# Kernel tuning notes

Hardware: AMD Instinct MI355X
Metric: run time of the kernel (lower is better)

## Reference

```python
import jax, jax.numpy as jnp
import numpy as np

O, NI, F, D, NN, M = 2048, 16, 4, 128, 8, 8  # outfits, item slots, factors, dim, neighbors, valid slots
D2 = D // 2

def lrelu(x):
    return jax.nn.leaky_relu(x, 0.01)

def mlp2(x, W1, b1, W2, b2):
    # Linear -> LeakyReLU -> Linear -> LeakyReLU (Dropout is identity at inference)
    return lrelu(lrelu(x @ W1 + b1) @ W2 + b2)

def setup_inputs():
    ks = jax.random.split(jax.random.key(0), 16)
    s = 0.05
    pos = jnp.arange(NI)[None, :]
    outfit_items = jnp.where(pos < M, jax.random.randint(ks[0], (O, NI), 0, NI), -1)
    items_neighbor = jax.random.randint(ks[1], (O, NI, NN), -1, NI)
    items_feature = jax.random.normal(ks[2], (O, NI, D), dtype=jnp.float32)
    items_factors = jnp.zeros((O, NI, F, D), dtype=jnp.float32)
    p = {
        'cf_W1': jax.random.normal(ks[3], (F, D, D2)) * s,
        'cf_b1': jnp.zeros((F, D2)),
        'cf_W2': jax.random.normal(ks[4], (F, D2, D)) * s,
        'cf_b2': jnp.zeros((F, D)),
        'f2f_W1': jax.random.normal(ks[5], (D, D)) * s, 'f2f_b1': jnp.zeros((D,)),
        'f2f_W2': jax.random.normal(ks[6], (D, D)) * s, 'f2f_b2': jnp.zeros((D,)),
        'f2i_W1': jax.random.normal(ks[7], (D, D)) * s, 'f2i_b1': jnp.zeros((D,)),
        'f2i_W2': jax.random.normal(ks[8], (D, D)) * s, 'f2i_b2': jnp.zeros((D,)),
        'i2i_W1': jax.random.normal(ks[9], (D, D)) * s, 'i2i_b1': jnp.zeros((D,)),
        'i2i_W2': jax.random.normal(ks[10], (D, D)) * s, 'i2i_b2': jnp.zeros((D,)),
        'o2s_W': jax.random.normal(ks[11], (D, 1)) * s, 'o2s_b': jnp.zeros((1,)),
    }
    return dict(outfit_items=outfit_items, items_feature=items_feature,
                items_neighbor=items_neighbor, items_factors=items_factors, **p)

def _forward(outfit_items, items_feature, items_neighbor, items_factors,
             cf_W1, cf_b1, cf_W2, cf_b2, f2f_W1, f2f_b1, f2f_W2, f2f_b2,
             f2i_W1, f2i_b1, f2i_W2, f2i_b2, i2i_W1, i2i_b1, i2i_W2, i2i_b2,
             o2s_W, o2s_b):
    del items_factors  # creat_factors overwrites every entry in the original
    # --- creat_factors: per-factor 2-layer MLP on every item feature -> [O,NI,F,D]
    h = lrelu(jnp.einsum('oid,fde->oife', items_feature, cf_W1) + cf_b1)
    fac = lrelu(jnp.einsum('oife,fed->oifd', h, cf_W2) + cf_b2)

    # --- inter_factors: sequential over outfit slots; later slots read updated factors
    def outfit_fac(fac_o, oi_o, nbr_o):
        def step(f, i):
            valid = i != -1
            ic = jnp.maximum(i, 0)
            cand = jnp.concatenate([oi_o, nbr_o[ic]])                # [NI+NN]
            cm = (cand != -1) & (cand != i) & valid
            t = f[ic]                                                # [F,D] snapshot
            msg = mlp2(t[None] * f[jnp.maximum(cand, 0)],
                       f2f_W1, f2f_b1, f2f_W2, f2f_b2)               # [NI+NN,F,D]
            add = jnp.sum(jnp.where(cm[:, None, None], msg, 0.0), axis=0)
            return f.at[ic].add(jnp.where(valid, add, 0.0)), None
        f, _ = jax.lax.scan(step, fac_o, oi_o)
        return f
    fac = jax.vmap(outfit_fac)(fac, outfit_items, items_neighbor)

    # --- infer_items: feature[i] += sum_j f2i(fac[i,j]) for outfit members
    g = mlp2(fac, f2i_W1, f2i_b1, f2i_W2, f2i_b2).sum(axis=2)        # [O,NI,D]
    ic = jnp.maximum(outfit_items, 0)
    w = (outfit_items != -1).astype(g.dtype)                          # [O,NI]
    gsel = jnp.take_along_axis(g, ic[..., None], axis=1)
    scat = jax.vmap(lambda gs, idx, ww: jnp.zeros((NI, D), gs.dtype).at[idx].add(ww[:, None] * gs))
    feat = items_feature + scat(gsel, ic, w)

    # --- inter_items: sequential; current value detached (.data in original)
    def outfit_feat(fo_init, oi_o):
        jc = jnp.maximum(oi_o, 0)
        def step(fo, i):
            valid = i != -1
            ic_ = jnp.maximum(i, 0)
            t = jax.lax.stop_gradient(fo[ic_])
            msgs = mlp2(fo[jc], i2i_W1, i2i_b1, i2i_W2, i2i_b2)      # [NI,D]
            m = ((oi_o != -1) & (oi_o != i)).astype(fo.dtype)
            new = t + jnp.sum(m[:, None] * msgs, axis=0)
            return jnp.where(valid, fo.at[ic_].set(new), fo), None
        fo, _ = jax.lax.scan(step, fo_init, oi_o)
        return fo
    feat = jax.vmap(outfit_feat)(feat, outfit_items)

    # --- infer_outfit + score
    fsel = jnp.take_along_axis(feat, ic[..., None], axis=1)
    outfits = jnp.sum(w[..., None] * fsel, axis=1)                    # [O,D]
    scores = jax.nn.sigmoid(outfits @ o2s_W + o2s_b)[:, 0]            # [O]

    # --- com_loss: ||F F^T - I||_F^2 over valid slots (positional mask), / n_outfits
    G = jnp.einsum('oifd,oigd->oifg', fac, fac) - jnp.eye(F, dtype=fac.dtype)
    com = jnp.sum(w * jnp.sum(G * G, axis=(-1, -2))) / O
    return scores, jnp.reshape(com, (1,))

def reference(outfit_items, items_feature, items_neighbor, items_factors,
              cf_W1, cf_b1, cf_W2, cf_b2, f2f_W1, f2f_b1, f2f_W2, f2f_b2,
              f2i_W1, f2i_b1, f2i_W2, f2i_b2, i2i_W1, i2i_b1, i2i_W2, i2i_b2,
              o2s_W, o2s_b):
    return _forward(outfit_items, items_feature, items_neighbor, items_factors,
                    cf_W1, cf_b1, cf_W2, cf_b2, f2f_W1, f2f_b1, f2f_W2, f2f_b2,
                    f2i_W1, f2i_b1, f2i_W2, f2i_b2, i2i_W1, i2i_b1, i2i_W2, i2i_b2,
                    o2s_W, o2s_b)
```

## Files before the change

### kernel.cpp

```cpp
#include <hip/hip_runtime.h>
#include <hip/hip_bf16.h>
#include <math.h>


typedef __attribute__((ext_vector_type(8))) short short8;
typedef __attribute__((ext_vector_type(4))) float f32x4;

#define MFMA16(a, b, c) __builtin_amdgcn_mfma_f32_16x16x32_bf16(a, b, c, 0, 0, 0)

__device__ __forceinline__ float lrelu(float x) { return fmaxf(x, 0.01f * x); }

__device__ __forceinline__ ushort f2bf(float f) {
  unsigned u = __builtin_bit_cast(unsigned, f);
  u += 0x7fffu + ((u >> 16) & 1u);
  return (ushort)(u >> 16);
}
__device__ __forceinline__ float bflo(unsigned u) {
  return __builtin_bit_cast(float, u << 16);
}
__device__ __forceinline__ unsigned pk2(float a, float b) {
  float2 t; t.x = a; t.y = b;
  __hip_bfloat162 h = __float22bfloat162_rn(t);
  unsigned u;
  __builtin_memcpy(&u, &h, 4);
  return u;
}


__global__ __launch_bounds__(256) void prep_weights(
    const float* __restrict__ cfW1, const float* __restrict__ cfW2,
    const float* __restrict__ f2fW1, const float* __restrict__ f2fW2,
    const float* __restrict__ f2iW1, const float* __restrict__ f2iW2,
    const float* __restrict__ i2iW1, const float* __restrict__ i2iW2,
    ushort* __restrict__ ws, float* __restrict__ out) {
  const int idx = (int)(blockIdx.x * 256 + threadIdx.x);
  if (idx == 0) out[2048] = 0.0f;
  float v;
  if (idx < 32768) {
    int f = idx >> 13, r = idx & 8191, n = r >> 7, k = r & 127;
    v = cfW1[f * 8192 + k * 64 + n];
  } else if (idx < 65536) {
    int t = idx - 32768;
    int f = t >> 13, r = t & 8191, n = r >> 6, k = r & 63;
    v = cfW2[f * 8192 + k * 128 + n];
  } else {
    int t = idx - 65536;
    int seg = t >> 14, r = t & 16383, n = r >> 7, k = r & 127;
    const float* W = (seg == 0) ? f2fW1 : (seg == 1) ? f2fW2 :
                     (seg == 2) ? f2iW1 : (seg == 3) ? f2iW2 :
                     (seg == 4) ? i2iW1 : i2iW2;
    v = W[k * 128 + n];
  }
  ws[idx] = f2bf(v);
}

__global__ __launch_bounds__(512, 4) void mfgn_kernel(
    const int* __restrict__ outfit_items,
    const float* __restrict__ items_feature,
    const int* __restrict__ items_neighbor,
    const float* __restrict__ cfb1, const float* __restrict__ cfb2,
    const float* __restrict__ f2fb1, const float* __restrict__ f2fb2,
    const float* __restrict__ f2ib1, const float* __restrict__ f2ib2,
    const float* __restrict__ i2ib1, const float* __restrict__ i2ib2,
    const float* __restrict__ o2sW, const float* __restrict__ o2sb,
    const ushort* __restrict__ wsW,
    float* __restrict__ out)
{
  __shared__ float facL[16 * 528];
  __shared__ ushort prodS[64 * 136] __attribute__((aligned(16)));
  __shared__ ushort hidS[64 * 136] __attribute__((aligned(16)));
  __shared__ ushort featB[16 * 136] __attribute__((aligned(16)));
  __shared__ float redE[8];
  __shared__ int oiL[16];
  __shared__ int clAll[256];
  __shared__ int ncAll[16];
  __shared__ int vslL[16];
  __shared__ int refcntL[16];
  __shared__ int nvsL;

  const int o = blockIdx.x;
  const int tid = (int)threadIdx.x;
  const int lane = tid & 63;
  const int wid = tid >> 6;
  const int n16 = lane & 15;
  const int q = lane >> 4;
  const int kb = q * 8;
  const int col = wid * 16 + n16;

  if (tid < 16) oiL[tid] = outfit_items[o * 16 + tid];
  {
    const int n = tid >> 5, d0 = (tid & 31) * 4;
    float4 v = *(const float4*)(items_feature + o * 2048 + tid * 4);
    uint2 pk; pk.x = pk2(v.x, v.y); pk.y = pk2(v.z, v.w);
    *(uint2*)(featB + n * 136 + d0) = pk;
  }
  if (tid == 0) {
    int cnt = 0;
    for (int s = 0; s < 16; ++s) refcntL[s] = 0;
    for (int s = 0; s < 16; ++s) {
      int v = oiL[s];
      if (v != -1) { vslL[cnt++] = s; refcntL[v]++; }
    }
    nvsL = cnt;
  }
  for (int s = wid; s < 16; s += 8) {
    const int iv = outfit_items[o * 16 + s];
    if (iv == -1) { if (lane == 0) ncAll[s] = 0; continue; }
    int cand = -1;
    if (lane < 24) cand = (lane < 16) ? outfit_items[o * 16 + lane]
                                      : items_neighbor[o * 128 + iv * 8 + (lane - 16)];
    bool ok = (lane < 24) && (cand != -1) && (cand != iv);
    unsigned long long bm = __ballot(ok);
    if (ok) clAll[s * 16 + __popcll(bm & ((1ull << lane) - 1ull))] = cand;
    if (lane == 0) ncAll[s] = (int)__popcll(bm);
  }
  __syncthreads();
  const int nvs = nvsL;

  {
    const int f = wid & 3, half = wid >> 2;
    short8 wA[2][4];
#pragma unroll
    for (int etl = 0; etl < 2; ++etl)
#pragma unroll
      for (int kt = 0; kt < 4; ++kt)
        wA[etl][kt] = *(const short8*)(wsW + (f * 64 + (half * 2 + etl) * 16 + n16) * 128
                                       + kt * 32 + kb);
    f32x4 acc[2];
#pragma unroll
    for (int etl = 0; etl < 2; ++etl)
      acc[etl] = *(const f32x4*)(cfb1 + f * 64 + (half * 2 + etl) * 16 + q * 4);
    for (int kt = 0; kt < 4; ++kt) {
      short8 x = *(const short8*)(featB + n16 * 136 + kt * 32 + kb);
      acc[0] = MFMA16(wA[0][kt], x, acc[0]);
      acc[1] = MFMA16(wA[1][kt], x, acc[1]);
    }
#pragma unroll
    for (int etl = 0; etl < 2; ++etl) {
      float h0 = lrelu(acc[etl][0]), h1 = lrelu(acc[etl][1]);
      float h2 = lrelu(acc[etl][2]), h3 = lrelu(acc[etl][3]);
      uint2 pk; pk.x = pk2(h0, h1); pk.y = pk2(h2, h3);
      *(uint2*)(hidS + (f * 16 + n16) * 136 + (half * 2 + etl) * 16 + q * 4) = pk;
    }
    __syncthreads();
    short8 wB[4][2];
#pragma unroll
    for (int ctl = 0; ctl < 4; ++ctl)
#pragma unroll
      for (int kt = 0; kt < 2; ++kt)
        wB[ctl][kt] = *(const short8*)(wsW + 32768 + (f * 128 + half * 64 + ctl * 16 + n16) * 64
                                       + kt * 32 + kb);
    f32x4 acc2[4];
#pragma unroll
    for (int ctl = 0; ctl < 4; ++ctl) {
      float b2 = cfb2[f * 128 + half * 64 + ctl * 16 + n16];
      acc2[ctl] = (f32x4){b2, b2, b2, b2};
    }
    for (int kt = 0; kt < 2; ++kt) {
      short8 h = *(const short8*)(hidS + (f * 16 + n16) * 136 + kt * 32 + kb);
#pragma unroll
      for (int ctl = 0; ctl < 4; ++ctl) acc2[ctl] = MFMA16(h, wB[ctl][kt], acc2[ctl]);
    }
#pragma unroll
    for (int ctl = 0; ctl < 4; ++ctl) {
      int c = half * 64 + ctl * 16 + n16;
#pragma unroll
      for (int r = 0; r < 4; ++r)
        facL[(q * 4 + r) * 528 + f * 132 + c] = lrelu(acc2[ctl][r]);
    }
    __syncthreads();
  }

  {
    short8 w1f[4], w2f[4];
#pragma unroll
    for (int kt = 0; kt < 4; ++kt) {
      w1f[kt] = *(const short8*)(wsW + 65536 + col * 128 + kt * 32 + kb);
      w2f[kt] = *(const short8*)(wsW + 81920 + col * 128 + kt * 32 + kb);
    }
    const f32x4 b1q = *(const f32x4*)(f2fb1 + wid * 16 + q * 4);
    const float b2v = f2fb2[col];
    const int rS = tid >> 3, kcS = tid & 7;
    const int fS = rS & 3, ciS = rS >> 2;
    const int k0 = kcS * 16;

    for (int u = 0; u < nvs; ++u) {
      const int s = vslL[u];
      const int iv = oiL[s];
      const int nc = ncAll[s];
      if (ciS < nc) {
        const int cit = clAll[s * 16 + ciS];
        const float* tp = facL + iv * 528 + fS * 132;
        const float* cp = facL + cit * 528 + fS * 132;
#pragma unroll
        for (int i2 = 0; i2 < 2; ++i2) {
          const int k = k0 + i2 * 8;
          float4 a0 = *(const float4*)(tp + k), a1 = *(const float4*)(tp + k + 4);
          float4 c0 = *(const float4*)(cp + k), c1 = *(const float4*)(cp + k + 4);
          uint4 u4;
          u4.x = pk2(a0.x * c0.x, a0.y * c0.y); u4.y = pk2(a0.z * c0.z, a0.w * c0.w);
          u4.z = pk2(a1.x * c1.x, a1.y * c1.y); u4.w = pk2(a1.z * c1.z, a1.w * c1.w);
          *(uint4*)(prodS + rS * 136 + k) = u4;
        }
      } else {
        uint4 z; z.x = z.y = z.z = z.w = 0;
        *(uint4*)(prodS + rS * 136 + k0) = z;
        *(uint4*)(prodS + rS * 136 + k0 + 8) = z;
      }
      __syncthreads();
      f32x4 acc[4];
#pragma unroll
      for (int mt = 0; mt < 4; ++mt) acc[mt] = b1q;
      for (int kt = 0; kt < 4; ++kt)
#pragma unroll
        for (int mt = 0; mt < 4; ++mt) {
          short8 x = *(const short8*)(prodS + (mt * 16 + n16) * 136 + kt * 32 + kb);
          acc[mt] = MFMA16(w1f[kt], x, acc[mt]);
        }
#pragma unroll
      for (int mt = 0; mt < 4; ++mt) {
        float h0 = lrelu(acc[mt][0]), h1 = lrelu(acc[mt][1]);
        float h2 = lrelu(acc[mt][2]), h3 = lrelu(acc[mt][3]);
        uint2 pk; pk.x = pk2(h0, h1); pk.y = pk2(h2, h3);
        *(uint2*)(hidS + (mt * 16 + n16) * 136 + wid * 16 + q * 4) = pk;
      }
      __syncthreads();
      f32x4 acc2[4];
#pragma unroll
      for (int mt = 0; mt < 4; ++mt) acc2[mt] = (f32x4){b2v, b2v, b2v, b2v};
      for (int kt = 0; kt < 4; ++kt)
#pragma unroll
        for (int mt = 0; mt < 4; ++mt) {
          short8 h = *(const short8*)(hidS + (mt * 16 + n16) * 136 + kt * 32 + kb);
          acc2[mt] = MFMA16(h, w2f[kt], acc2[mt]);
        }
      float part[4] = {0.f, 0.f, 0.f, 0.f};
#pragma unroll
      for (int mt = 0; mt < 4; ++mt) {
        bool act = (mt * 4 + q) < nc;
        if (act) {
#pragma unroll
          for (int r = 0; r < 4; ++r) part[r] += lrelu(acc2[mt][r]);
        }
      }
#pragma unroll
      for (int r = 0; r < 4; ++r) {
        float v = part[r];
        v += __shfl_xor(v, 16);
        v += __shfl_xor(v, 32);
        part[r] = v;
      }
      if (q == 0) {
#pragma unroll
        for (int r = 0; r < 4; ++r)
          facL[iv * 528 + r * 132 + col] += part[r];
      }
      __syncthreads();
    }
  }

  {
    short8 w1f[4], w2f[4];
#pragma unroll
    for (int kt = 0; kt < 4; ++kt) {
      w1f[kt] = *(const short8*)(wsW + 98304 + col * 128 + kt * 32 + kb);
      w2f[kt] = *(const short8*)(wsW + 114688 + col * 128 + kt * 32 + kb);
    }
    const f32x4 b1q = *(const f32x4*)(f2ib1 + wid * 16 + q * 4);
    const float b2v = f2ib2[col];
    {
      const int r = tid >> 3, kc = tid & 7, k0 = kc * 16;
      const int f = r & 3, item = r >> 2;
      const float* sp = facL + item * 528 + f * 132;
#pragma unroll
      for (int i2 = 0; i2 < 2; ++i2) {
        const int k = k0 + i2 * 8;
        float4 a0 = *(const float4*)(sp + k), a1 = *(const float4*)(sp + k + 4);
        uint4 u;
        u.x = pk2(a0.x, a0.y); u.y = pk2(a0.z, a0.w);
        u.z = pk2(a1.x, a1.y); u.w = pk2(a1.z, a1.w);
        *(uint4*)(prodS + r * 136 + k) = u;
      }
    }
    __syncthreads();
    f32x4 acc[4];
#pragma unroll
    for (int mt = 0; mt < 4; ++mt) acc[mt] = b1q;
    for (int kt = 0; kt < 4; ++kt)
#pragma unroll
      for (int mt = 0; mt < 4; ++mt) {
        short8 x = *(const short8*)(prodS + (mt * 16 + n16) * 136 + kt * 32 + kb);
        acc[mt] = MFMA16(w1f[kt], x, acc[mt]);
      }
#pragma unroll
    for (int mt = 0; mt < 4; ++mt) {
      float h0 = lrelu(acc[mt][0]), h1 = lrelu(acc[mt][1]);
      float h2 = lrelu(acc[mt][2]), h3 = lrelu(acc[mt][3]);
      uint2 pk; pk.x = pk2(h0, h1); pk.y = pk2(h2, h3);
      *(uint2*)(hidS + (mt * 16 + n16) * 136 + wid * 16 + q * 4) = pk;
    }
    __syncthreads();
    f32x4 acc2[4];
#pragma unroll
    for (int mt = 0; mt < 4; ++mt) acc2[mt] = (f32x4){b2v, b2v, b2v, b2v};
    for (int kt = 0; kt < 4; ++kt)
#pragma unroll
      for (int mt = 0; mt < 4; ++mt) {
        short8 h = *(const short8*)(hidS + (mt * 16 + n16) * 136 + kt * 32 + kb);
        acc2[mt] = MFMA16(h, w2f[kt], acc2[mt]);
      }
#pragma unroll
    for (int mt = 0; mt < 4; ++mt) {
      int item = mt * 4 + q;
      float g = 0.f;
#pragma unroll
      for (int r = 0; r < 4; ++r) g += lrelu(acc2[mt][r]);
      int a = item * 136 + col;
      featB[a] = f2bf(bflo((unsigned)featB[a]) + (float)refcntL[item] * g);
    }
    __syncthreads();
  }

  {
    short8 w1f[4], w2f[4];
#pragma unroll
    for (int kt = 0; kt < 4; ++kt) {
      w1f[kt] = *(const short8*)(wsW + 131072 + col * 128 + kt * 32 + kb);
      w2f[kt] = *(const short8*)(wsW + 147456 + col * 128 + kt * 32 + kb);
    }
    const f32x4 b1q = *(const f32x4*)(i2ib1 + wid * 16 + q * 4);
    const float b2v = i2ib2[col];

    for (int u = 0; u < nvs; ++u) {
      const int iv = oiL[vslL[u]];
      f32x4 acc = b1q;
      for (int kt = 0; kt < 4; ++kt) {
        short8 x = *(const short8*)(featB + n16 * 136 + kt * 32 + kb);
        acc = MFMA16(w1f[kt], x, acc);
      }
      {
        float h0 = lrelu(acc[0]), h1 = lrelu(acc[1]);
        float h2 = lrelu(acc[2]), h3 = lrelu(acc[3]);
        uint2 pk; pk.x = pk2(h0, h1); pk.y = pk2(h2, h3);
        *(uint2*)(hidS + n16 * 136 + wid * 16 + q * 4) = pk;
      }
      __syncthreads();
      f32x4 acc2 = (f32x4){b2v, b2v, b2v, b2v};
      for (int kt = 0; kt < 4; ++kt) {
        short8 h = *(const short8*)(hidS + n16 * 136 + kt * 32 + kb);
        acc2 = MFMA16(h, w2f[kt], acc2);
      }
      float part = 0.f;
#pragma unroll
      for (int r = 0; r < 4; ++r) {
        int item = q * 4 + r;
        float w = (item == iv) ? 0.0f : (float)refcntL[item];
        part += w * lrelu(acc2[r]);
      }
      part += __shfl_xor(part, 16);
      part += __shfl_xor(part, 32);
      if (q == 0) {
        int a = iv * 136 + col;
        featB[a] = f2bf(bflo((unsigned)featB[a]) + part);
      }
      __syncthreads();
    }
  }

  if (tid < 128) {
    float sum = 0.0f;
    for (int u = 0; u < nvs; ++u)
      sum += bflo((unsigned)featB[oiL[vslL[u]] * 136 + tid]);
    float v = sum * o2sW[tid];
#pragma unroll
    for (int off = 1; off < 64; off <<= 1) v += __shfl_xor(v, off);
    if (lane == 0) redE[wid] = v;
  }
  __syncthreads();
  if (tid == 0) {
    float t = redE[0] + redE[1] + o2sb[0];
    out[o] = 1.0f / (1.0f + expf(-t));
  }

  {
    const int n = tid >> 5, f = (tid >> 3) & 3, g = (tid >> 1) & 3, h = tid & 1;
    const float* pa = facL + n * 528 + f * 132 + h * 64;
    const float* pb = facL + n * 528 + g * 132 + h * 64;
    float dot = 0.0f;
    for (int i = 0; i < 16; ++i) {
      float4 a = *(const float4*)(pa + i * 4);
      float4 b = *(const float4*)(pb + i * 4);
      dot += a.x * b.x + a.y * b.y + a.z * b.z + a.w * b.w;
    }
    dot += __shfl_xor(dot, 1);
    float v = dot - ((f == g) ? 1.0f : 0.0f);
    float sq = (h == 0 && oiL[n] != -1) ? v * v : 0.0f;
#pragma unroll
    for (int off = 1; off < 64; off <<= 1) sq += __shfl_xor(sq, off);
    __syncthreads();
    if (lane == 0) redE[wid] = sq;
    __syncthreads();
    if (tid == 0) {
      float tot = 0.f;
#pragma unroll
      for (int w = 0; w < 8; ++w) tot += redE[w];
      atomicAdd(out + 2048, tot * (1.0f / 2048.0f));
    }
  }
}

extern "C" void kernel_launch(void* const* d_in, const int* in_sizes, int n_in,
                              void* d_out, int out_size, void* d_ws, size_t ws_size,
                              hipStream_t stream) {
  float* out = (float*)d_out;
  ushort* ws = (ushort*)d_ws;
  hipLaunchKernelGGL(prep_weights, dim3(640), dim3(256), 0, stream,
                     (const float*)d_in[4], (const float*)d_in[6],
                     (const float*)d_in[8], (const float*)d_in[10],
                     (const float*)d_in[12], (const float*)d_in[14],
                     (const float*)d_in[16], (const float*)d_in[18],
                     ws, out);
  hipLaunchKernelGGL(mfgn_kernel, dim3(2048), dim3(512), 0, stream,
                     (const int*)d_in[0],
                     (const float*)d_in[1],
                     (const int*)d_in[2],
                     (const float*)d_in[5], (const float*)d_in[7],
                     (const float*)d_in[9], (const float*)d_in[11],
                     (const float*)d_in[13], (const float*)d_in[15],
                     (const float*)d_in[17], (const float*)d_in[19],
                     (const float*)d_in[20], (const float*)d_in[21],
                     (const ushort*)ws,
                     out);
}
```

Before: 337.2 us.

## Shrink LDS footprint with XOR-swizzled unpadded buffers and merge prod/hidden buffers

Replaces the padded shared-memory layouts with unpadded rows indexed through an XOR swizzle, so bank conflicts stay avoided without padding. It merges the separate product and hidden staging buffers into one and adds barriers to guard the reuse. The neighbor list is stored as bytes, and launch bounds now ask for more resident blocks per CU. The aim is to cut LDS use so more workgroups fit per CU, at the cost of two extra barriers per loop iteration. Zero-filling of unused product rows is also dropped, so those rows feed stale data into columns that are later masked out.

```diff
diff --git a/kernel.cpp b/kernel.cpp
--- a/kernel.cpp
+++ b/kernel.cpp
@@ -24,6 +24,13 @@
   unsigned u;
   __builtin_memcpy(&u, &h, 4);
   return u;
+}
+
+__device__ __forceinline__ int fIdx(int row, int k) {
+  return row * 128 + (k ^ ((row & 7) << 2));
+}
+__device__ __forceinline__ int bIdx(int row, int k) {
+  return row * 128 + (k ^ ((row & 7) << 3));
 }
 
 
@@ -54,7 +61,7 @@
   ws[idx] = f2bf(v);
 }
 
-__global__ __launch_bounds__(512, 4) void mfgn_kernel(
+__global__ __launch_bounds__(512, 6) void mfgn_kernel(
     const int* __restrict__ outfit_items,
     const float* __restrict__ items_feature,
     const int* __restrict__ items_neighbor,
@@ -66,13 +73,12 @@
     const ushort* __restrict__ wsW,
     float* __restrict__ out)
 {
-  __shared__ float facL[16 * 528];
-  __shared__ ushort prodS[64 * 136] __attribute__((aligned(16)));
-  __shared__ ushort hidS[64 * 136] __attribute__((aligned(16)));
-  __shared__ ushort featB[16 * 136] __attribute__((aligned(16)));
+  __shared__ float facL[64 * 128] __attribute__((aligned(16)));
+  __shared__ ushort bufS[64 * 128] __attribute__((aligned(16)));
+  __shared__ ushort featB[16 * 128] __attribute__((aligned(16)));
   __shared__ float redE[8];
   __shared__ int oiL[16];
-  __shared__ int clAll[256];
+  __shared__ unsigned char clAllU[256];
   __shared__ int ncAll[16];
   __shared__ int vslL[16];
   __shared__ int refcntL[16];
@@ -92,7 +98,7 @@
     const int n = tid >> 5, d0 = (tid & 31) * 4;
     float4 v = *(const float4*)(items_feature + o * 2048 + tid * 4);
     uint2 pk; pk.x = pk2(v.x, v.y); pk.y = pk2(v.z, v.w);
-    *(uint2*)(featB + n * 136 + d0) = pk;
+    *(uint2*)(featB + bIdx(n, d0)) = pk;
   }
   if (tid == 0) {
     int cnt = 0;
@@ -111,7 +117,7 @@
                                       : items_neighbor[o * 128 + iv * 8 + (lane - 16)];
     bool ok = (lane < 24) && (cand != -1) && (cand != iv);
     unsigned long long bm = __ballot(ok);
-    if (ok) clAll[s * 16 + __popcll(bm & ((1ull << lane) - 1ull))] = cand;
+    if (ok) clAllU[s * 16 + __popcll(bm & ((1ull << lane) - 1ull))] = (unsigned char)cand;
     if (lane == 0) ncAll[s] = (int)__popcll(bm);
   }
   __syncthreads();
@@ -131,7 +137,7 @@
     for (int etl = 0; etl < 2; ++etl)
       acc[etl] = *(const f32x4*)(cfb1 + f * 64 + (half * 2 + etl) * 16 + q * 4);
     for (int kt = 0; kt < 4; ++kt) {
-      short8 x = *(const short8*)(featB + n16 * 136 + kt * 32 + kb);
+      short8 x = *(const short8*)(featB + bIdx(n16, kt * 32 + kb));
       acc[0] = MFMA16(wA[0][kt], x, acc[0]);
       acc[1] = MFMA16(wA[1][kt], x, acc[1]);
     }
@@ -140,7 +146,7 @@
       float h0 = lrelu(acc[etl][0]), h1 = lrelu(acc[etl][1]);
       float h2 = lrelu(acc[etl][2]), h3 = lrelu(acc[etl][3]);
       uint2 pk; pk.x = pk2(h0, h1); pk.y = pk2(h2, h3);
-      *(uint2*)(hidS + (f * 16 + n16) * 136 + (half * 2 + etl) * 16 + q * 4) = pk;
+      *(uint2*)(bufS + bIdx(f * 16 + n16, (half * 2 + etl) * 16 + q * 4)) = pk;
     }
     __syncthreads();
     short8 wB[4][2];
@@ -157,7 +163,7 @@
       acc2[ctl] = (f32x4){b2, b2, b2, b2};
     }
     for (int kt = 0; kt < 2; ++kt) {
-      short8 h = *(const short8*)(hidS + (f * 16 + n16) * 136 + kt * 32 + kb);
+      short8 h = *(const short8*)(bufS + bIdx(f * 16 + n16, kt * 32 + kb));
 #pragma unroll
       for (int ctl = 0; ctl < 4; ++ctl) acc2[ctl] = MFMA16(h, wB[ctl][kt], acc2[ctl]);
     }
@@ -166,7 +172,7 @@
       int c = half * 64 + ctl * 16 + n16;
 #pragma unroll
       for (int r = 0; r < 4; ++r)
-        facL[(q * 4 + r) * 528 + f * 132 + c] = lrelu(acc2[ctl][r]);
+        facL[fIdx((q * 4 + r) * 4 + f, c)] = lrelu(acc2[ctl][r]);
     }
     __syncthreads();
   }
@@ -189,23 +195,23 @@
       const int iv = oiL[s];
       const int nc = ncAll[s];
       if (ciS < nc) {
-        const int cit = clAll[s * 16 + ciS];
-        const float* tp = facL + iv * 528 + fS * 132;
-        const float* cp = facL + cit * 528 + fS * 132;
+        const int cit = (int)clAllU[s * 16 + ciS];
+        const int rT = iv * 4 + fS, rC = cit * 4 + fS;
+        const int swT = (rT & 7) << 2, swC = (rC & 7) << 2;
+        const float* tp = facL + rT * 128;
+        const float* cp = facL + rC * 128;
 #pragma unroll
         for (int i2 = 0; i2 < 2; ++i2) {
           const int k = k0 + i2 * 8;
-          float4 a0 = *(const float4*)(tp + k), a1 = *(const float4*)(tp + k + 4);
-          float4 c0 = *(const float4*)(cp + k), c1 = *(const float4*)(cp + k + 4);
+          float4 a0 = *(const float4*)(tp + (k ^ swT));
+          float4 a1 = *(const float4*)(tp + ((k + 4) ^ swT));
+          float4 c0 = *(const float4*)(cp + (k ^ swC));
+          float4 c1 = *(const float4*)(cp + ((k + 4) ^ swC));
           uint4 u4;
           u4.x = pk2(a0.x * c0.x, a0.y * c0.y); u4.y = pk2(a0.z * c0.z, a0.w * c0.w);
           u4.z = pk2(a1.x * c1.x, a1.y * c1.y); u4.w = pk2(a1.z * c1.z, a1.w * c1.w);
-          *(uint4*)(prodS + rS * 136 + k) = u4;
+          *(uint4*)(bufS + bIdx(rS, k)) = u4;
         }
-      } else {
-        uint4 z; z.x = z.y = z.z = z.w = 0;
-        *(uint4*)(prodS + rS * 136 + k0) = z;
-        *(uint4*)(prodS + rS * 136 + k0 + 8) = z;
       }
       __syncthreads();
       f32x4 acc[4];
@@ -214,15 +220,16 @@
       for (int kt = 0; kt < 4; ++kt)
 #pragma unroll
         for (int mt = 0; mt < 4; ++mt) {
-          short8 x = *(const short8*)(prodS + (mt * 16 + n16) * 136 + kt * 32 + kb);
+          short8 x = *(const short8*)(bufS + bIdx(mt * 16 + n16, kt * 32 + kb));
           acc[mt] = MFMA16(w1f[kt], x, acc[mt]);
         }
+      __syncthreads();
 #pragma unroll
       for (int mt = 0; mt < 4; ++mt) {
         float h0 = lrelu(acc[mt][0]), h1 = lrelu(acc[mt][1]);
         float h2 = lrelu(acc[mt][2]), h3 = lrelu(acc[mt][3]);
         uint2 pk; pk.x = pk2(h0, h1); pk.y = pk2(h2, h3);
-        *(uint2*)(hidS + (mt * 16 + n16) * 136 + wid * 16 + q * 4) = pk;
+        *(uint2*)(bufS + bIdx(mt * 16 + n16, wid * 16 + q * 4)) = pk;
       }
       __syncthreads();
       f32x4 acc2[4];
@@ -231,7 +238,7 @@
       for (int kt = 0; kt < 4; ++kt)
 #pragma unroll
         for (int mt = 0; mt < 4; ++mt) {
-          short8 h = *(const short8*)(hidS + (mt * 16 + n16) * 136 + kt * 32 + kb);
+          short8 h = *(const short8*)(bufS + bIdx(mt * 16 + n16, kt * 32 + kb));
           acc2[mt] = MFMA16(h, w2f[kt], acc2[mt]);
         }
       float part[4] = {0.f, 0.f, 0.f, 0.f};
@@ -253,7 +260,7 @@
       if (q == 0) {
 #pragma unroll
         for (int r = 0; r < 4; ++r)
-          facL[iv * 528 + r * 132 + col] += part[r];
+          facL[fIdx(iv * 4 + r, col)] += part[r];
       }
       __syncthreads();
     }
@@ -270,16 +277,17 @@
     const float b2v = f2ib2[col];
     {
       const int r = tid >> 3, kc = tid & 7, k0 = kc * 16;
-      const int f = r & 3, item = r >> 2;
-      const float* sp = facL + item * 528 + f * 132;
+      const int sw = (r & 7) << 2;
+      const float* sp = facL + r * 128;
 #pragma unroll
       for (int i2 = 0; i2 < 2; ++i2) {
         const int k = k0 + i2 * 8;
-        float4 a0 = *(const float4*)(sp + k), a1 = *(const float4*)(sp + k + 4);
+        float4 a0 = *(const float4*)(sp + (k ^ sw));
+        float4 a1 = *(const float4*)(sp + ((k + 4) ^ sw));
         uint4 u;
         u.x = pk2(a0.x, a0.y); u.y = pk2(a0.z, a0.w);
         u.z = pk2(a1.x, a1.y); u.w = pk2(a1.z, a1.w);
-        *(uint4*)(prodS + r * 136 + k) = u;
+        *(uint4*)(bufS + bIdx(r, k)) = u;
       }
     }
     __syncthreads();
@@ -289,15 +297,16 @@
     for (int kt = 0; kt < 4; ++kt)
 #pragma unroll
       for (int mt = 0; mt < 4; ++mt) {
-        short8 x = *(const short8*)(prodS + (mt * 16 + n16) * 136 + kt * 32 + kb);
+        short8 x = *(const short8*)(bufS + bIdx(mt * 16 + n16, kt * 32 + kb));
         acc[mt] = MFMA16(w1f[kt], x, acc[mt]);
       }
+    __syncthreads();
 #pragma unroll
     for (int mt = 0; mt < 4; ++mt) {
       float h0 = lrelu(acc[mt][0]), h1 = lrelu(acc[mt][1]);
       float h2 = lrelu(acc[mt][2]), h3 = lrelu(acc[mt][3]);
       uint2 pk; pk.x = pk2(h0, h1); pk.y = pk2(h2, h3);
-      *(uint2*)(hidS + (mt * 16 + n16) * 136 + wid * 16 + q * 4) = pk;
+      *(uint2*)(bufS + bIdx(mt * 16 + n16, wid * 16 + q * 4)) = pk;
     }
     __syncthreads();
     f32x4 acc2[4];
@@ -306,7 +315,7 @@
     for (int kt = 0; kt < 4; ++kt)
 #pragma unroll
       for (int mt = 0; mt < 4; ++mt) {
-        short8 h = *(const short8*)(hidS + (mt * 16 + n16) * 136 + kt * 32 + kb);
+        short8 h = *(const short8*)(bufS + bIdx(mt * 16 + n16, kt * 32 + kb));
         acc2[mt] = MFMA16(h, w2f[kt], acc2[mt]);
       }
 #pragma unroll
@@ -315,7 +324,7 @@
       float g = 0.f;
 #pragma unroll
       for (int r = 0; r < 4; ++r) g += lrelu(acc2[mt][r]);
-      int a = item * 136 + col;
+      int a = bIdx(item, col);
       featB[a] = f2bf(bflo((unsigned)featB[a]) + (float)refcntL[item] * g);
     }
     __syncthreads();
@@ -335,19 +344,19 @@
       const int iv = oiL[vslL[u]];
       f32x4 acc = b1q;
       for (int kt = 0; kt < 4; ++kt) {
-        short8 x = *(const short8*)(featB + n16 * 136 + kt * 32 + kb);
+        short8 x = *(const short8*)(featB + bIdx(n16, kt * 32 + kb));
         acc = MFMA16(w1f[kt], x, acc);
       }
       {
         float h0 = lrelu(acc[0]), h1 = lrelu(acc[1]);
         float h2 = lrelu(acc[2]), h3 = lrelu(acc[3]);
         uint2 pk; pk.x = pk2(h0, h1); pk.y = pk2(h2, h3);
-        *(uint2*)(hidS + n16 * 136 + wid * 16 + q * 4) = pk;
+        *(uint2*)(bufS + bIdx(n16, wid * 16 + q * 4)) = pk;
       }
       __syncthreads();
       f32x4 acc2 = (f32x4){b2v, b2v, b2v, b2v};
       for (int kt = 0; kt < 4; ++kt) {
-        short8 h = *(const short8*)(hidS + n16 * 136 + kt * 32 + kb);
+        short8 h = *(const short8*)(bufS + bIdx(n16, kt * 32 + kb));
         acc2 = MFMA16(h, w2f[kt], acc2);
       }
       float part = 0.f;
@@ -360,7 +369,7 @@
       part += __shfl_xor(part, 16);
       part += __shfl_xor(part, 32);
       if (q == 0) {
-        int a = iv * 136 + col;
+        int a = bIdx(iv, col);
         featB[a] = f2bf(bflo((unsigned)featB[a]) + part);
       }
       __syncthreads();
@@ -369,8 +378,10 @@
 
   if (tid < 128) {
     float sum = 0.0f;
-    for (int u = 0; u < nvs; ++u)
-      sum += bflo((unsigned)featB[oiL[vslL[u]] * 136 + tid]);
+    for (int u = 0; u < nvs; ++u) {
+      int it = oiL[vslL[u]];
+      sum += bflo((unsigned)featB[bIdx(it, tid)]);
+    }
     float v = sum * o2sW[tid];
 #pragma unroll
     for (int off = 1; off < 64; off <<= 1) v += __shfl_xor(v, off);
@@ -384,12 +395,15 @@
 
   {
     const int n = tid >> 5, f = (tid >> 3) & 3, g = (tid >> 1) & 3, h = tid & 1;
-    const float* pa = facL + n * 528 + f * 132 + h * 64;
-    const float* pb = facL + n * 528 + g * 132 + h * 64;
+    const int rA = n * 4 + f, rB = n * 4 + g;
+    const int swA = (rA & 7) << 2, swB = (rB & 7) << 2;
+    const float* pa = facL + rA * 128;
+    const float* pb = facL + rB * 128;
     float dot = 0.0f;
     for (int i = 0; i < 16; ++i) {
-      float4 a = *(const float4*)(pa + i * 4);
-      float4 b = *(const float4*)(pb + i * 4);
+      const int k = h * 64 + i * 4;
+      float4 a = *(const float4*)(pa + (k ^ swA));
+      float4 b = *(const float4*)(pb + (k ^ swB));
       dot += a.x * b.x + a.y * b.y + a.z * b.z + a.w * b.w;
     }
     dot += __shfl_xor(dot, 1);
```

Result: slower. 397.2 us (+17.8%).

## Retile f2f/f2i MLP MFMAs to 32x32 per wave and trim redundant work

Applied to the files above, without the earlier changes.

Switches the f2f and f2i MLP stages from each wave owning 16 output columns across all 64 rows to a 2x4 wave grid where each wave owns 32 rows by 32 columns. Each loaded LDS fragment now feeds two MFMAs instead of one, which cuts LDS reads. It also drops the zero-fill of unused prodS rows, caches the i2i input fragments in registers and refreshes only the updated row, and computes only the upper triangle of the symmetric Gram matrix with doubled off-diagonal weight. In exchange, the per-wave partial sums into facL now need LDS atomics, register pressure rises, and the occupancy hint drops from 4 to 2 blocks. Skipping the zero-fill leaves stale data in inactive rows, which is harmless only because those rows are masked when summed.

```diff
diff --git a/kernel.cpp b/kernel.cpp
--- a/kernel.cpp
+++ b/kernel.cpp
@@ -54,7 +54,7 @@
   ws[idx] = f2bf(v);
 }
 
-__global__ __launch_bounds__(512, 4) void mfgn_kernel(
+__global__ __launch_bounds__(512, 2) void mfgn_kernel(
     const int* __restrict__ outfit_items,
     const float* __restrict__ items_feature,
     const int* __restrict__ items_neighbor,
@@ -86,6 +86,8 @@
   const int q = lane >> 4;
   const int kb = q * 8;
   const int col = wid * 16 + n16;
+  const int colp = wid & 3, mtp = wid >> 2;
+  const int cb0 = colp * 32;
 
   if (tid < 16) oiL[tid] = outfit_items[o * 16 + tid];
   {
@@ -172,14 +174,21 @@
   }
 
   {
-    short8 w1f[4], w2f[4];
-#pragma unroll
-    for (int kt = 0; kt < 4; ++kt) {
-      w1f[kt] = *(const short8*)(wsW + 65536 + col * 128 + kt * 32 + kb);
-      w2f[kt] = *(const short8*)(wsW + 81920 + col * 128 + kt * 32 + kb);
-    }
-    const f32x4 b1q = *(const f32x4*)(f2fb1 + wid * 16 + q * 4);
-    const float b2v = f2fb2[col];
+    short8 w1f[2][4], w2f[2][4];
+#pragma unroll
+    for (int c2 = 0; c2 < 2; ++c2)
+#pragma unroll
+      for (int kt = 0; kt < 4; ++kt) {
+        w1f[c2][kt] = *(const short8*)(wsW + 65536 + (cb0 + c2 * 16 + n16) * 128 + kt * 32 + kb);
+        w2f[c2][kt] = *(const short8*)(wsW + 81920 + (cb0 + c2 * 16 + n16) * 128 + kt * 32 + kb);
+      }
+    f32x4 b1q[2];
+    float b2v[2];
+#pragma unroll
+    for (int c2 = 0; c2 < 2; ++c2) {
+      b1q[c2] = *(const f32x4*)(f2fb1 + cb0 + c2 * 16 + q * 4);
+      b2v[c2] = f2fb2[cb0 + c2 * 16 + n16];
+    }
     const int rS = tid >> 3, kcS = tid & 7;
     const int fS = rS & 3, ciS = rS >> 2;
     const int k0 = kcS * 16;
@@ -202,72 +211,92 @@
           u4.z = pk2(a1.x * c1.x, a1.y * c1.y); u4.w = pk2(a1.z * c1.z, a1.w * c1.w);
           *(uint4*)(prodS + rS * 136 + k) = u4;
         }
-      } else {
-        uint4 z; z.x = z.y = z.z = z.w = 0;
-        *(uint4*)(prodS + rS * 136 + k0) = z;
-        *(uint4*)(prodS + rS * 136 + k0 + 8) = z;
       }
       __syncthreads();
-      f32x4 acc[4];
-#pragma unroll
-      for (int mt = 0; mt < 4; ++mt) acc[mt] = b1q;
-      for (int kt = 0; kt < 4; ++kt)
-#pragma unroll
-        for (int mt = 0; mt < 4; ++mt) {
-          short8 x = *(const short8*)(prodS + (mt * 16 + n16) * 136 + kt * 32 + kb);
-          acc[mt] = MFMA16(w1f[kt], x, acc[mt]);
+      f32x4 acc00 = b1q[0], acc01 = b1q[1], acc10 = b1q[0], acc11 = b1q[1];
+      for (int kt = 0; kt < 4; ++kt) {
+        short8 x0 = *(const short8*)(prodS + (mtp * 32 + n16) * 136 + kt * 32 + kb);
+        short8 x1 = *(const short8*)(prodS + (mtp * 32 + 16 + n16) * 136 + kt * 32 + kb);
+        acc00 = MFMA16(w1f[0][kt], x0, acc00);
+        acc01 = MFMA16(w1f[1][kt], x0, acc01);
+        acc10 = MFMA16(w1f[0][kt], x1, acc10);
+        acc11 = MFMA16(w1f[1][kt], x1, acc11);
+      }
+      {
+        uint2 pk;
+        pk.x = pk2(lrelu(acc00[0]), lrelu(acc00[1])); pk.y = pk2(lrelu(acc00[2]), lrelu(acc00[3]));
+        *(uint2*)(hidS + (mtp * 32 + n16) * 136 + cb0 + q * 4) = pk;
+        pk.x = pk2(lrelu(acc01[0]), lrelu(acc01[1])); pk.y = pk2(lrelu(acc01[2]), lrelu(acc01[3]));
+        *(uint2*)(hidS + (mtp * 32 + n16) * 136 + cb0 + 16 + q * 4) = pk;
+        pk.x = pk2(lrelu(acc10[0]), lrelu(acc10[1])); pk.y = pk2(lrelu(acc10[2]), lrelu(acc10[3]));
+        *(uint2*)(hidS + (mtp * 32 + 16 + n16) * 136 + cb0 + q * 4) = pk;
+        pk.x = pk2(lrelu(acc11[0]), lrelu(acc11[1])); pk.y = pk2(lrelu(acc11[2]), lrelu(acc11[3]));
+        *(uint2*)(hidS + (mtp * 32 + 16 + n16) * 136 + cb0 + 16 + q * 4) = pk;
+      }
+      __syncthreads();
+      f32x4 a200 = (f32x4){b2v[0], b2v[0], b2v[0], b2v[0]};
+      f32x4 a201 = (f32x4){b2v[1], b2v[1], b2v[1], b2v[1]};
+      f32x4 a210 = (f32x4){b2v[0], b2v[0], b2v[0], b2v[0]};
+      f32x4 a211 = (f32x4){b2v[1], b2v[1], b2v[1], b2v[1]};
+      for (int kt = 0; kt < 4; ++kt) {
+        short8 h0 = *(const short8*)(hidS + (mtp * 32 + n16) * 136 + kt * 32 + kb);
+        short8 h1 = *(const short8*)(hidS + (mtp * 32 + 16 + n16) * 136 + kt * 32 + kb);
+        a200 = MFMA16(h0, w2f[0][kt], a200);
+        a201 = MFMA16(h0, w2f[1][kt], a201);
+        a210 = MFMA16(h1, w2f[0][kt], a210);
+        a211 = MFMA16(h1, w2f[1][kt], a211);
+      }
+      const bool act0 = (mtp * 8 + q) < nc;
+      const bool act1 = (mtp * 8 + 4 + q) < nc;
+      float pr[2][4];
+#pragma unroll
+      for (int c2 = 0; c2 < 2; ++c2)
+#pragma unroll
+        for (int r = 0; r < 4; ++r) pr[c2][r] = 0.f;
+      if (act0) {
+#pragma unroll
+        for (int r = 0; r < 4; ++r) { pr[0][r] += lrelu(a200[r]); pr[1][r] += lrelu(a201[r]); }
+      }
+      if (act1) {
+#pragma unroll
+        for (int r = 0; r < 4; ++r) { pr[0][r] += lrelu(a210[r]); pr[1][r] += lrelu(a211[r]); }
+      }
+#pragma unroll
+      for (int c2 = 0; c2 < 2; ++c2)
+#pragma unroll
+        for (int r = 0; r < 4; ++r) {
+          float v = pr[c2][r];
+          v += __shfl_xor(v, 16);
+          v += __shfl_xor(v, 32);
+          pr[c2][r] = v;
         }
-#pragma unroll
-      for (int mt = 0; mt < 4; ++mt) {
-        float h0 = lrelu(acc[mt][0]), h1 = lrelu(acc[mt][1]);
-        float h2 = lrelu(acc[mt][2]), h3 = lrelu(acc[mt][3]);
-        uint2 pk; pk.x = pk2(h0, h1); pk.y = pk2(h2, h3);
-        *(uint2*)(hidS + (mt * 16 + n16) * 136 + wid * 16 + q * 4) = pk;
+      if (q == 0) {
+#pragma unroll
+        for (int c2 = 0; c2 < 2; ++c2)
+#pragma unroll
+          for (int r = 0; r < 4; ++r)
+            atomicAdd(&facL[iv * 528 + r * 132 + cb0 + c2 * 16 + n16], pr[c2][r]);
       }
       __syncthreads();
-      f32x4 acc2[4];
-#pragma unroll
-      for (int mt = 0; mt < 4; ++mt) acc2[mt] = (f32x4){b2v, b2v, b2v, b2v};
-      for (int kt = 0; kt < 4; ++kt)
-#pragma unroll
-        for (int mt = 0; mt < 4; ++mt) {
-          short8 h = *(const short8*)(hidS + (mt * 16 + n16) * 136 + kt * 32 + kb);
-          acc2[mt] = MFMA16(h, w2f[kt], acc2[mt]);
-        }
-      float part[4] = {0.f, 0.f, 0.f, 0.f};
-#pragma unroll
-      for (int mt = 0; mt < 4; ++mt) {
-        bool act = (mt * 4 + q) < nc;
-        if (act) {
-#pragma unroll
-          for (int r = 0; r < 4; ++r) part[r] += lrelu(acc2[mt][r]);
-        }
-      }
-#pragma unroll
-      for (int r = 0; r < 4; ++r) {
-        float v = part[r];
-        v += __shfl_xor(v, 16);
-        v += __shfl_xor(v, 32);
-        part[r] = v;
-      }
-      if (q == 0) {
-#pragma unroll
-        for (int r = 0; r < 4; ++r)
-          facL[iv * 528 + r * 132 + col] += part[r];
-      }
-      __syncthreads();
-    }
-  }
-
-  {
-    short8 w1f[4], w2f[4];
-#pragma unroll
-    for (int kt = 0; kt < 4; ++kt) {
-      w1f[kt] = *(const short8*)(wsW + 98304 + col * 128 + kt * 32 + kb);
-      w2f[kt] = *(const short8*)(wsW + 114688 + col * 128 + kt * 32 + kb);
-    }
-    const f32x4 b1q = *(const f32x4*)(f2ib1 + wid * 16 + q * 4);
-    const float b2v = f2ib2[col];
+    }
+  }
+
+  {
+    short8 w1f[2][4], w2f[2][4];
+#pragma unroll
+    for (int c2 = 0; c2 < 2; ++c2)
+#pragma unroll
+      for (int kt = 0; kt < 4; ++kt) {
+        w1f[c2][kt] = *(const short8*)(wsW + 98304 + (cb0 + c2 * 16 + n16) * 128 + kt * 32 + kb);
+        w2f[c2][kt] = *(const short8*)(wsW + 114688 + (cb0 + c2 * 16 + n16) * 128 + kt * 32 + kb);
+      }
+    f32x4 b1q[2];
+    float b2v[2];
+#pragma unroll
+    for (int c2 = 0; c2 < 2; ++c2) {
+      b1q[c2] = *(const f32x4*)(f2ib1 + cb0 + c2 * 16 + q * 4);
+      b2v[c2] = f2ib2[cb0 + c2 * 16 + n16];
+    }
     {
       const int r = tid >> 3, kc = tid & 7, k0 = kc * 16;
       const int f = r & 3, item = r >> 2;
@@ -283,40 +312,51 @@
       }
     }
     __syncthreads();
-    f32x4 acc[4];
-#pragma unroll
-    for (int mt = 0; mt < 4; ++mt) acc[mt] = b1q;
-    for (int kt = 0; kt < 4; ++kt)
-#pragma unroll
-      for (int mt = 0; mt < 4; ++mt) {
-        short8 x = *(const short8*)(prodS + (mt * 16 + n16) * 136 + kt * 32 + kb);
-        acc[mt] = MFMA16(w1f[kt], x, acc[mt]);
-      }
-#pragma unroll
-    for (int mt = 0; mt < 4; ++mt) {
-      float h0 = lrelu(acc[mt][0]), h1 = lrelu(acc[mt][1]);
-      float h2 = lrelu(acc[mt][2]), h3 = lrelu(acc[mt][3]);
-      uint2 pk; pk.x = pk2(h0, h1); pk.y = pk2(h2, h3);
-      *(uint2*)(hidS + (mt * 16 + n16) * 136 + wid * 16 + q * 4) = pk;
-    }
-    __syncthreads();
-    f32x4 acc2[4];
-#pragma unroll
-    for (int mt = 0; mt < 4; ++mt) acc2[mt] = (f32x4){b2v, b2v, b2v, b2v};
-    for (int kt = 0; kt < 4; ++kt)
-#pragma unroll
-      for (int mt = 0; mt < 4; ++mt) {
-        short8 h = *(const short8*)(hidS + (mt * 16 + n16) * 136 + kt * 32 + kb);
-        acc2[mt] = MFMA16(h, w2f[kt], acc2[mt]);
-      }
-#pragma unroll
-    for (int mt = 0; mt < 4; ++mt) {
-      int item = mt * 4 + q;
-      float g = 0.f;
-#pragma unroll
-      for (int r = 0; r < 4; ++r) g += lrelu(acc2[mt][r]);
-      int a = item * 136 + col;
-      featB[a] = f2bf(bflo((unsigned)featB[a]) + (float)refcntL[item] * g);
+    f32x4 acc00 = b1q[0], acc01 = b1q[1], acc10 = b1q[0], acc11 = b1q[1];
+    for (int kt = 0; kt < 4; ++kt) {
+      short8 x0 = *(const short8*)(prodS + (mtp * 32 + n16) * 136 + kt * 32 + kb);
+      short8 x1 = *(const short8*)(prodS + (mtp * 32 + 16 + n16) * 136 + kt * 32 + kb);
+      acc00 = MFMA16(w1f[0][kt], x0, acc00);
+      acc01 = MFMA16(w1f[1][kt], x0, acc01);
+      acc10 = MFMA16(w1f[0][kt], x1, acc10);
+      acc11 = MFMA16(w1f[1][kt], x1, acc11);
+    }
+    {
+      uint2 pk;
+      pk.x = pk2(lrelu(acc00[0]), lrelu(acc00[1])); pk.y = pk2(lrelu(acc00[2]), lrelu(acc00[3]));
+      *(uint2*)(hidS + (mtp * 32 + n16) * 136 + cb0 + q * 4) = pk;
+      pk.x = pk2(lrelu(acc01[0]), lrelu(acc01[1])); pk.y = pk2(lrelu(acc01[2]), lrelu(acc01[3]));
+      *(uint2*)(hidS + (mtp * 32 + n16) * 136 + cb0 + 16 + q * 4) = pk;
+      pk.x = pk2(lrelu(acc10[0]), lrelu(acc10[1])); pk.y = pk2(lrelu(acc10[2]), lrelu(acc10[3]));
+      *(uint2*)(hidS + (mtp * 32 + 16 + n16) * 136 + cb0 + q * 4) = pk;
+      pk.x = pk2(lrelu(acc11[0]), lrelu(acc11[1])); pk.y = pk2(lrelu(acc11[2]), lrelu(acc11[3]));
+      *(uint2*)(hidS + (mtp * 32 + 16 + n16) * 136 + cb0 + 16 + q * 4) = pk;
+    }
+    __syncthreads();
+    f32x4 a200 = (f32x4){b2v[0], b2v[0], b2v[0], b2v[0]};
+    f32x4 a201 = (f32x4){b2v[1], b2v[1], b2v[1], b2v[1]};
+    f32x4 a210 = (f32x4){b2v[0], b2v[0], b2v[0], b2v[0]};
+    f32x4 a211 = (f32x4){b2v[1], b2v[1], b2v[1], b2v[1]};
+    for (int kt = 0; kt < 4; ++kt) {
+      short8 h0 = *(const short8*)(hidS + (mtp * 32 + n16) * 136 + kt * 32 + kb);
+      short8 h1 = *(const short8*)(hidS + (mtp * 32 + 16 + n16) * 136 + kt * 32 + kb);
+      a200 = MFMA16(h0, w2f[0][kt], a200);
+      a201 = MFMA16(h0, w2f[1][kt], a201);
+      a210 = MFMA16(h1, w2f[0][kt], a210);
+      a211 = MFMA16(h1, w2f[1][kt], a211);
+    }
+    {
+      const int it0 = mtp * 8 + q, it1 = mtp * 8 + 4 + q;
+      float g00 = lrelu(a200[0]) + lrelu(a200[1]) + lrelu(a200[2]) + lrelu(a200[3]);
+      float g01 = lrelu(a201[0]) + lrelu(a201[1]) + lrelu(a201[2]) + lrelu(a201[3]);
+      float g10 = lrelu(a210[0]) + lrelu(a210[1]) + lrelu(a210[2]) + lrelu(a210[3]);
+      float g11 = lrelu(a211[0]) + lrelu(a211[1]) + lrelu(a211[2]) + lrelu(a211[3]);
+      int a00 = it0 * 136 + cb0 + n16, a01 = it0 * 136 + cb0 + 16 + n16;
+      int a10 = it1 * 136 + cb0 + n16, a11 = it1 * 136 + cb0 + 16 + n16;
+      featB[a00] = f2bf(bflo((unsigned)featB[a00]) + (float)refcntL[it0] * g00);
+      featB[a01] = f2bf(bflo((unsigned)featB[a01]) + (float)refcntL[it0] * g01);
+      featB[a10] = f2bf(bflo((unsigned)featB[a10]) + (float)refcntL[it1] * g10);
+      featB[a11] = f2bf(bflo((unsigned)featB[a11]) + (float)refcntL[it1] * g11);
     }
     __syncthreads();
   }
@@ -330,14 +370,15 @@
     }
     const f32x4 b1q = *(const f32x4*)(i2ib1 + wid * 16 + q * 4);
     const float b2v = i2ib2[col];
+    short8 xc[4];
+#pragma unroll
+    for (int kt = 0; kt < 4; ++kt)
+      xc[kt] = *(const short8*)(featB + n16 * 136 + kt * 32 + kb);
 
     for (int u = 0; u < nvs; ++u) {
       const int iv = oiL[vslL[u]];
       f32x4 acc = b1q;
-      for (int kt = 0; kt < 4; ++kt) {
-        short8 x = *(const short8*)(featB + n16 * 136 + kt * 32 + kb);
-        acc = MFMA16(w1f[kt], x, acc);
-      }
+      for (int kt = 0; kt < 4; ++kt) acc = MFMA16(w1f[kt], xc[kt], acc);
       {
         float h0 = lrelu(acc[0]), h1 = lrelu(acc[1]);
         float h2 = lrelu(acc[2]), h3 = lrelu(acc[3]);
@@ -364,6 +405,11 @@
         featB[a] = f2bf(bflo((unsigned)featB[a]) + part);
       }
       __syncthreads();
+      if (n16 == iv) {
+#pragma unroll
+        for (int kt = 0; kt < 4; ++kt)
+          xc[kt] = *(const short8*)(featB + n16 * 136 + kt * 32 + kb);
+      }
     }
   }
 
@@ -384,17 +430,20 @@
 
   {
     const int n = tid >> 5, f = (tid >> 3) & 3, g = (tid >> 1) & 3, h = tid & 1;
-    const float* pa = facL + n * 528 + f * 132 + h * 64;
-    const float* pb = facL + n * 528 + g * 132 + h * 64;
     float dot = 0.0f;
-    for (int i = 0; i < 16; ++i) {
-      float4 a = *(const float4*)(pa + i * 4);
-      float4 b = *(const float4*)(pb + i * 4);
-      dot += a.x * b.x + a.y * b.y + a.z * b.z + a.w * b.w;
+    if (f <= g) {
+      const float* pa = facL + n * 528 + f * 132 + h * 64;
+      const float* pb = facL + n * 528 + g * 132 + h * 64;
+      for (int i = 0; i < 16; ++i) {
+        float4 a = *(const float4*)(pa + i * 4);
+        float4 b = *(const float4*)(pb + i * 4);
+        dot += a.x * b.x + a.y * b.y + a.z * b.z + a.w * b.w;
+      }
     }
     dot += __shfl_xor(dot, 1);
     float v = dot - ((f == g) ? 1.0f : 0.0f);
-    float sq = (h == 0 && oiL[n] != -1) ? v * v : 0.0f;
+    float wgt = (f == g) ? 1.0f : 2.0f;
+    float sq = (h == 0 && f <= g && oiL[n] != -1) ? wgt * v * v : 0.0f;
 #pragma unroll
     for (int off = 1; off < 64; off <<= 1) sq += __shfl_xor(sq, off);
     __syncthreads();
```

Result: slower. 520.3 us (+54.3%).

## Prefetch next product staging into loop tail, cache i2i inputs, halve Gram work

Applied to the files above, without the earlier changes.

The f2f loop now builds the product tile for the next valid slot, or the f2i input tile after the last slot, before the loop-ending barrier, which removes one block-wide sync per iteration. Staging is remapped so each wave covers a 16-column slice for all 64 rows, and rows without a neighbour are no longer zeroed. The i2i loop keeps its featB MFMA operands in registers and reloads only the row that was updated. The Gram loss computes only the upper triangle and doubles the off-diagonal terms, and the occupancy hint in launch bounds drops from 4 to 2. Skipping the zero fill relies on MFMA outputs for inactive rows being masked later, and the lower occupancy hint allows more registers per thread.

```diff
diff --git a/kernel.cpp b/kernel.cpp
--- a/kernel.cpp
+++ b/kernel.cpp
@@ -54,7 +54,7 @@
   ws[idx] = f2bf(v);
 }
 
-__global__ __launch_bounds__(512, 4) void mfgn_kernel(
+__global__ __launch_bounds__(512, 2) void mfgn_kernel(
     const int* __restrict__ outfit_items,
     const float* __restrict__ items_feature,
     const int* __restrict__ items_neighbor,
@@ -86,6 +86,8 @@
   const int q = lane >> 4;
   const int kb = q * 8;
   const int col = wid * 16 + n16;
+  const int fS = lane & 3, ciS = lane >> 2;
+  const int kc0 = wid * 16;
 
   if (tid < 16) oiL[tid] = outfit_items[o * 16 + tid];
   {
@@ -180,34 +182,42 @@
     }
     const f32x4 b1q = *(const f32x4*)(f2fb1 + wid * 16 + q * 4);
     const float b2v = f2fb2[col];
-    const int rS = tid >> 3, kcS = tid & 7;
-    const int fS = rS & 3, ciS = rS >> 2;
-    const int k0 = kcS * 16;
+
+    auto stageB = [&](int s, int iv_, int nc_) {
+      if (ciS < nc_) {
+        const int cit = clAll[s * 16 + ciS];
+        const float* tp = facL + iv_ * 528 + fS * 132 + kc0;
+        const float* cp = facL + cit * 528 + fS * 132 + kc0;
+#pragma unroll
+        for (int i2 = 0; i2 < 2; ++i2) {
+          float4 a0 = *(const float4*)(tp + i2 * 8), a1 = *(const float4*)(tp + i2 * 8 + 4);
+          float4 c0 = *(const float4*)(cp + i2 * 8), c1 = *(const float4*)(cp + i2 * 8 + 4);
+          uint4 u4;
+          u4.x = pk2(a0.x * c0.x, a0.y * c0.y); u4.y = pk2(a0.z * c0.z, a0.w * c0.w);
+          u4.z = pk2(a1.x * c1.x, a1.y * c1.y); u4.w = pk2(a1.z * c1.z, a1.w * c1.w);
+          *(uint4*)(prodS + lane * 136 + kc0 + i2 * 8) = u4;
+        }
+      }
+    };
+    auto stageC = [&]() {
+      const float* sp = facL + ciS * 528 + fS * 132 + kc0;
+#pragma unroll
+      for (int i2 = 0; i2 < 2; ++i2) {
+        float4 a0 = *(const float4*)(sp + i2 * 8), a1 = *(const float4*)(sp + i2 * 8 + 4);
+        uint4 u4;
+        u4.x = pk2(a0.x, a0.y); u4.y = pk2(a0.z, a0.w);
+        u4.z = pk2(a1.x, a1.y); u4.w = pk2(a1.z, a1.w);
+        *(uint4*)(prodS + lane * 136 + kc0 + i2 * 8) = u4;
+      }
+    };
+
+    if (nvs > 0) { const int s0 = vslL[0]; stageB(s0, oiL[s0], ncAll[s0]); }
+    __syncthreads();
 
     for (int u = 0; u < nvs; ++u) {
       const int s = vslL[u];
       const int iv = oiL[s];
       const int nc = ncAll[s];
-      if (ciS < nc) {
-        const int cit = clAll[s * 16 + ciS];
-        const float* tp = facL + iv * 528 + fS * 132;
-        const float* cp = facL + cit * 528 + fS * 132;
-#pragma unroll
-        for (int i2 = 0; i2 < 2; ++i2) {
-          const int k = k0 + i2 * 8;
-          float4 a0 = *(const float4*)(tp + k), a1 = *(const float4*)(tp + k + 4);
-          float4 c0 = *(const float4*)(cp + k), c1 = *(const float4*)(cp + k + 4);
-          uint4 u4;
-          u4.x = pk2(a0.x * c0.x, a0.y * c0.y); u4.y = pk2(a0.z * c0.z, a0.w * c0.w);
-          u4.z = pk2(a1.x * c1.x, a1.y * c1.y); u4.w = pk2(a1.z * c1.z, a1.w * c1.w);
-          *(uint4*)(prodS + rS * 136 + k) = u4;
-        }
-      } else {
-        uint4 z; z.x = z.y = z.z = z.w = 0;
-        *(uint4*)(prodS + rS * 136 + k0) = z;
-        *(uint4*)(prodS + rS * 136 + k0 + 8) = z;
-      }
-      __syncthreads();
       f32x4 acc[4];
 #pragma unroll
       for (int mt = 0; mt < 4; ++mt) acc[mt] = b1q;
@@ -255,8 +265,15 @@
         for (int r = 0; r < 4; ++r)
           facL[iv * 528 + r * 132 + col] += part[r];
       }
+      if (u + 1 < nvs) {
+        const int s2 = vslL[u + 1];
+        stageB(s2, oiL[s2], ncAll[s2]);
+      } else {
+        stageC();
+      }
       __syncthreads();
     }
+    if (nvs == 0) { stageC(); __syncthreads(); }
   }
 
   {
@@ -268,21 +285,6 @@
     }
     const f32x4 b1q = *(const f32x4*)(f2ib1 + wid * 16 + q * 4);
     const float b2v = f2ib2[col];
-    {
-      const int r = tid >> 3, kc = tid & 7, k0 = kc * 16;
-      const int f = r & 3, item = r >> 2;
-      const float* sp = facL + item * 528 + f * 132;
-#pragma unroll
-      for (int i2 = 0; i2 < 2; ++i2) {
-        const int k = k0 + i2 * 8;
-        float4 a0 = *(const float4*)(sp + k), a1 = *(const float4*)(sp + k + 4);
-        uint4 u;
-        u.x = pk2(a0.x, a0.y); u.y = pk2(a0.z, a0.w);
-        u.z = pk2(a1.x, a1.y); u.w = pk2(a1.z, a1.w);
-        *(uint4*)(prodS + r * 136 + k) = u;
-      }
-    }
-    __syncthreads();
     f32x4 acc[4];
 #pragma unroll
     for (int mt = 0; mt < 4; ++mt) acc[mt] = b1q;
@@ -330,14 +332,15 @@
     }
     const f32x4 b1q = *(const f32x4*)(i2ib1 + wid * 16 + q * 4);
     const float b2v = i2ib2[col];
+    short8 xc[4];
+#pragma unroll
+    for (int kt = 0; kt < 4; ++kt)
+      xc[kt] = *(const short8*)(featB + n16 * 136 + kt * 32 + kb);
 
     for (int u = 0; u < nvs; ++u) {
       const int iv = oiL[vslL[u]];
       f32x4 acc = b1q;
-      for (int kt = 0; kt < 4; ++kt) {
-        short8 x = *(const short8*)(featB + n16 * 136 + kt * 32 + kb);
-        acc = MFMA16(w1f[kt], x, acc);
-      }
+      for (int kt = 0; kt < 4; ++kt) acc = MFMA16(w1f[kt], xc[kt], acc);
       {
         float h0 = lrelu(acc[0]), h1 = lrelu(acc[1]);
         float h2 = lrelu(acc[2]), h3 = lrelu(acc[3]);
@@ -364,6 +367,11 @@
         featB[a] = f2bf(bflo((unsigned)featB[a]) + part);
       }
       __syncthreads();
+      if (n16 == iv) {
+#pragma unroll
+        for (int kt = 0; kt < 4; ++kt)
+          xc[kt] = *(const short8*)(featB + n16 * 136 + kt * 32 + kb);
+      }
     }
   }
 
@@ -384,17 +392,20 @@
 
   {
     const int n = tid >> 5, f = (tid >> 3) & 3, g = (tid >> 1) & 3, h = tid & 1;
-    const float* pa = facL + n * 528 + f * 132 + h * 64;
-    const float* pb = facL + n * 528 + g * 132 + h * 64;
     float dot = 0.0f;
-    for (int i = 0; i < 16; ++i) {
-      float4 a = *(const float4*)(pa + i * 4);
-      float4 b = *(const float4*)(pb + i * 4);
-      dot += a.x * b.x + a.y * b.y + a.z * b.z + a.w * b.w;
+    if (f <= g) {
+      const float* pa = facL + n * 528 + f * 132 + h * 64;
+      const float* pb = facL + n * 528 + g * 132 + h * 64;
+      for (int i = 0; i < 16; ++i) {
+        float4 a = *(const float4*)(pa + i * 4);
+        float4 b = *(const float4*)(pb + i * 4);
+        dot += a.x * b.x + a.y * b.y + a.z * b.z + a.w * b.w;
+      }
     }
     dot += __shfl_xor(dot, 1);
     float v = dot - ((f == g) ? 1.0f : 0.0f);
-    float sq = (h == 0 && oiL[n] != -1) ? v * v : 0.0f;
+    float wgt = (f == g) ? 1.0f : 2.0f;
+    float sq = (h == 0 && f <= g && oiL[n] != -1) ? wgt * v * v : 0.0f;
 #pragma unroll
     for (int off = 1; off < 64; off <<= 1) sq += __shfl_xor(sq, off);
     __syncthreads();
```

New measurement: 336.5 us. No clear change (-0.2%).
